# Kernel tuning notes

Measured on AMD Instinct MI355X. Metric: run time of the kernel, lower is better.

## Reference

```python
import jax, jax.numpy as jnp
import numpy as np

WORLD_SIZE = 8
M_LOCAL = 1024   # max_M // world_size
K = 4096
N = 4096


def setup_inputs() -> dict:
    key = jax.random.key(0)
    k1, k2 = jax.random.split(key)
    # Each rank's local activation shard: [world_size, M_local, K]
    A_shards = jax.random.normal(k1, (WORLD_SIZE, M_LOCAL, K), dtype=jnp.float32)
    # weight stored [N, K] (transed_weight = False path)
    weight = jax.random.normal(k2, (N, K), dtype=jnp.float32) * 0.02
    return {"A_shards": A_shards, "weight": weight, "transed_weight": 0}


def reference(A_shards, weight, transed_weight):
    # All-gather: concatenate rank shards along M -> [max_M, K]
    ws, m_local, k = A_shards.shape
    A_full = A_shards.reshape(ws * m_local, k)
    # GEMM: weight is [N, K] when transed_weight is falsy, [K, N] otherwise
    W = weight if transed_weight else weight.T  # -> [K, N]
    out = jnp.matmul(A_full, W)  # [max_M, N]
    return out
```

## Files before the change

### kernel.cpp

```cpp
#include <hip/hip_runtime.h>
#include <hip/hip_bf16.h>

#define M_TOTAL 8192
#define KDIM    4096
#define NDIM    4096

#define BM 256
#define BN 256
#define BK 32
#define NT (KDIM / BK)
#define AREG (BM * BK)
#define BREG (BN * BK)
#define BUFE (AREG + BREG)

typedef __bf16 bf16x8 __attribute__((ext_vector_type(8)));
typedef float  f32x4  __attribute__((ext_vector_type(4)));

__device__ __forceinline__ unsigned short f32_to_bf16_rne(unsigned u) {
    unsigned r = u + 0x7fffu + ((u >> 16) & 1u);
    return (unsigned short)(r >> 16);
}

__device__ __forceinline__ void cvt8(const float* __restrict__ s,
                                     unsigned short* __restrict__ d) {
    const uint4* sp = (const uint4*)s;
    uint4 x = sp[0];
    uint4 y = sp[1];
    uint4 o;
    o.x = (unsigned)f32_to_bf16_rne(x.x) | ((unsigned)f32_to_bf16_rne(x.y) << 16);
    o.y = (unsigned)f32_to_bf16_rne(x.z) | ((unsigned)f32_to_bf16_rne(x.w) << 16);
    o.z = (unsigned)f32_to_bf16_rne(y.x) | ((unsigned)f32_to_bf16_rne(y.y) << 16);
    o.w = (unsigned)f32_to_bf16_rne(y.z) | ((unsigned)f32_to_bf16_rne(y.w) << 16);
    *(uint4*)d = o;
}

__global__ __launch_bounds__(256) void cvt_both(const float* __restrict__ A,
                                                unsigned short* __restrict__ Abf,
                                                long nA,
                                                const float* __restrict__ W,
                                                unsigned short* __restrict__ Wbf) {
    long i = ((long)blockIdx.x * 256 + threadIdx.x) * 8;
    if (i < nA) {
        cvt8(A + i, Abf + i);
    } else {
        long j = i - nA;
        cvt8(W + j, Wbf + j);
    }
}

__device__ __forceinline__ void gload_lds16(const unsigned short* g, unsigned short* l) {
    __builtin_amdgcn_global_load_lds(
        (const __attribute__((address_space(1))) unsigned int*)g,
        (__attribute__((address_space(3))) unsigned int*)l,
        16, 0, 0);
}

__global__ __launch_bounds__(512, 2) void gemm_bt(const unsigned short* __restrict__ A,
                                                  const unsigned short* __restrict__ B,
                                                  float* __restrict__ C) {
    extern __shared__ unsigned short smem[];

    const int tid  = threadIdx.x;
    const int wave = tid >> 6;
    const int lane = tid & 63;

    const int n0 = blockIdx.x * BN;
    const int m0 = blockIdx.y * BM;

    const int rsub = tid >> 2;
    const int cswz = (tid & 3) ^ ((tid >> 3) & 3);
    const unsigned short* pA0 = A + (size_t)(m0 + rsub)       * KDIM + cswz * 8;
    const unsigned short* pA1 = A + (size_t)(m0 + 128 + rsub) * KDIM + cswz * 8;
    const unsigned short* pB0 = B + (size_t)(n0 + rsub)       * KDIM + cswz * 8;
    const unsigned short* pB1 = B + (size_t)(n0 + 128 + rsub) * KDIM + cswz * 8;
    const int woff = wave * 512;

    const int wm   = wave >> 2;
    const int wn   = wave & 3;
    const int quad = lane >> 4;
    const int r    = lane & 15;
    const int sidx = (quad ^ ((r >> 1) & 3)) * 8;

    int aoff[8], boff[4];
#pragma unroll
    for (int mi = 0; mi < 8; ++mi) aoff[mi] = (wm * 128 + mi * 16 + r) * BK + sidx;
#pragma unroll
    for (int ni = 0; ni < 4; ++ni) boff[ni] = (wn * 64 + ni * 16 + r) * BK + sidx;

    f32x4 acc[8][4] = {};

#define SAp(b) (smem + (b) * BUFE)
#define SBq(b) (smem + (b) * BUFE + AREG)
#define STAGE(TS, SB) do {                                                  \
        const size_t so_ = (size_t)(TS) * BK;                               \
        gload_lds16(pA0 + so_, SAp(SB) + woff);                             \
        gload_lds16(pA1 + so_, SAp(SB) + 4096 + woff);                      \
        gload_lds16(pB0 + so_, SBq(SB) + woff);                             \
        gload_lds16(pB1 + so_, SBq(SB) + 4096 + woff);                      \
    } while (0)

    STAGE(0, 0);
    STAGE(1, 1);
    STAGE(2, 2);

#define GITER(RB, SB, VM, DOSTAGE, TS) do {                                 \
        asm volatile("s_waitcnt vmcnt(" #VM ")" ::: "memory");              \
        __builtin_amdgcn_s_barrier();                                       \
        asm volatile("" ::: "memory");                                      \
        if (DOSTAGE) STAGE(TS, SB);                                         \
        bf16x8 aF[8], bF[4];                                                \
        _Pragma("unroll")                                                   \
        for (int mi = 0; mi < 8; ++mi)                                      \
            aF[mi] = *(const bf16x8*)(SAp(RB) + aoff[mi]);                  \
        _Pragma("unroll")                                                   \
        for (int ni = 0; ni < 4; ++ni)                                      \
            bF[ni] = *(const bf16x8*)(SBq(RB) + boff[ni]);                  \
        __builtin_amdgcn_s_setprio(1);                                      \
        _Pragma("unroll")                                                   \
        for (int mi = 0; mi < 8; ++mi)                                      \
            _Pragma("unroll")                                               \
            for (int ni = 0; ni < 4; ++ni)                                  \
                acc[mi][ni] = __builtin_amdgcn_mfma_f32_16x16x32_bf16(      \
                    aF[mi], bF[ni], acc[mi][ni], 0, 0, 0);                  \
        __builtin_amdgcn_s_setprio(0);                                      \
        asm volatile("s_waitcnt lgkmcnt(0)" ::: "memory");                  \
        __builtin_amdgcn_s_barrier();                                       \
        asm volatile("" ::: "memory");                                      \
    } while (0)

    for (int g = 0; g < NT / 4 - 1; ++g) {
        const int t = g * 4;
        GITER(0, 3, 8, true, t + 3);
        GITER(1, 0, 8, true, t + 4);
        GITER(2, 1, 8, true, t + 5);
        GITER(3, 2, 8, true, t + 6);
    }
    GITER(0, 3, 8, true, 127);
    GITER(1, 0, 8, false, 0);
    GITER(2, 1, 4, false, 0);
    GITER(3, 2, 0, false, 0);

#undef GITER
#undef STAGE
#undef SAp
#undef SBq

#pragma unroll
    for (int mi = 0; mi < 8; ++mi) {
        const int row = m0 + wm * 128 + mi * 16 + quad * 4;
#pragma unroll
        for (int ni = 0; ni < 4; ++ni) {
            const int col = n0 + wn * 64 + ni * 16 + r;
            float* p = C + (size_t)row * NDIM + col;
#pragma unroll
            for (int rr = 0; rr < 4; ++rr)
                p[(size_t)rr * NDIM] = acc[mi][ni][rr];
        }
    }
}

extern "C" void kernel_launch(void* const* d_in, const int* in_sizes, int n_in,
                              void* d_out, int out_size, void* d_ws, size_t ws_size,
                              hipStream_t stream) {
    const float* A = (const float*)d_in[0];
    const float* W = (const float*)d_in[1];
    float* out = (float*)d_out;

    unsigned short* Abf = (unsigned short*)d_ws;
    unsigned short* Wbf = Abf + (size_t)M_TOTAL * KDIM;

    const long nA = (long)M_TOTAL * KDIM;
    const long nW = (long)NDIM * KDIM;
    const long nTot = nA + nW;

    cvt_both<<<(int)(nTot / 8 / 256), 256, 0, stream>>>(A, Abf, nA, W, Wbf);

    static bool attr_done = false;
    if (!attr_done) {
        hipFuncSetAttribute((const void*)gemm_bt,
                            hipFuncAttributeMaxDynamicSharedMemorySize, 128 * 1024);
        attr_done = true;
    }

    dim3 grid(NDIM / BN, M_TOTAL / BM);
    gemm_bt<<<grid, 512, 128 * 1024, stream>>>(Abf, Wbf, out);
}
```

Before: 497.5 us.

## Split each K-tile into two half-phases interleaving LDS reads, global loads and MFMAs

Restructures the main loop so each K-step runs as two phases. Each phase loads half of the A fragments, issues half of the next stage's global-to-LDS loads, and runs a 4x4 block of MFMAs, with barriers between phases. The aim is a ping-pong schedule where LDS traffic and global loads overlap with matrix-core work, and fewer fragment registers are live at once. The cost is twice as many barriers per tile and changed vmcnt accounting in the tail, which could cause stalls or a subtle race if the wait counts are wrong.

```diff
diff --git a/kernel.cpp b/kernel.cpp
--- a/kernel.cpp
+++ b/kernel.cpp
@@ -88,6 +88,7 @@
     for (int ni = 0; ni < 4; ++ni) boff[ni] = (wn * 64 + ni * 16 + r) * BK + sidx;
 
     f32x4 acc[8][4] = {};
+    bf16x8 aFa[4], aFb[4], bF[4];
 
 #define SAp(b) (smem + (b) * BUFE)
 #define SBq(b) (smem + (b) * BUFE + AREG)
@@ -99,48 +100,78 @@
         gload_lds16(pB1 + so_, SBq(SB) + 4096 + woff);                      \
     } while (0)
 
+#define TILE(RB, SB, VM, DOSTAGE, TS) do {                                  \
+          \
+        _Pragma("unroll")                                                   \
+        for (int ni = 0; ni < 4; ++ni)                                      \
+            bF[ni] = *(const bf16x8*)(SBq(RB) + boff[ni]);                  \
+        _Pragma("unroll")                                                   \
+        for (int mi = 0; mi < 4; ++mi)                                      \
+            aFa[mi] = *(const bf16x8*)(SAp(RB) + aoff[mi]);                 \
+        if (DOSTAGE) {                                                      \
+            const size_t so_ = (size_t)(TS) * BK;                           \
+            gload_lds16(pA0 + so_, SAp(SB) + woff);                         \
+            gload_lds16(pA1 + so_, SAp(SB) + 4096 + woff);                  \
+        }                                                                   \
+        asm volatile("" ::: "memory");                                      \
+        __builtin_amdgcn_s_barrier();                                       \
+        asm volatile("s_waitcnt lgkmcnt(0)" ::: "memory");                  \
+        __builtin_amdgcn_s_setprio(1);                                      \
+        _Pragma("unroll")                                                   \
+        for (int mi = 0; mi < 4; ++mi)                                      \
+            _Pragma("unroll")                                               \
+            for (int ni = 0; ni < 4; ++ni)                                  \
+                acc[mi][ni] = __builtin_amdgcn_mfma_f32_16x16x32_bf16(      \
+                    aFa[mi], bF[ni], acc[mi][ni], 0, 0, 0);                 \
+        __builtin_amdgcn_s_setprio(0);                                      \
+        asm volatile("" ::: "memory");                                      \
+        __builtin_amdgcn_s_barrier();                                       \
+        asm volatile("" ::: "memory");                                      \
+        \
+        _Pragma("unroll")                                                   \
+        for (int mi = 0; mi < 4; ++mi)                                      \
+            aFb[mi] = *(const bf16x8*)(SAp(RB) + aoff[4 + mi]);             \
+        if (DOSTAGE) {                                                      \
+            const size_t so_ = (size_t)(TS) * BK;                           \
+            gload_lds16(pB0 + so_, SBq(SB) + woff);                         \
+            gload_lds16(pB1 + so_, SBq(SB) + 4096 + woff);                  \
+        }                                                                   \
+        asm volatile("s_waitcnt vmcnt(" #VM ")" ::: "memory");              \
+        __builtin_amdgcn_s_barrier();                                       \
+        asm volatile("s_waitcnt lgkmcnt(0)" ::: "memory");                  \
+        __builtin_amdgcn_s_setprio(1);                                      \
+        _Pragma("unroll")                                                   \
+        for (int mi = 0; mi < 4; ++mi)                                      \
+            _Pragma("unroll")                                               \
+            for (int ni = 0; ni < 4; ++ni)                                  \
+                acc[4 + mi][ni] = __builtin_amdgcn_mfma_f32_16x16x32_bf16(  \
+                    aFb[mi], bF[ni], acc[4 + mi][ni], 0, 0, 0);             \
+        __builtin_amdgcn_s_setprio(0);                                      \
+        asm volatile("" ::: "memory");                                      \
+        __builtin_amdgcn_s_barrier();                                       \
+        asm volatile("" ::: "memory");                                      \
+    } while (0)
+
     STAGE(0, 0);
     STAGE(1, 1);
     STAGE(2, 2);
-
-#define GITER(RB, SB, VM, DOSTAGE, TS) do {                                 \
-        asm volatile("s_waitcnt vmcnt(" #VM ")" ::: "memory");              \
-        __builtin_amdgcn_s_barrier();                                       \
-        asm volatile("" ::: "memory");                                      \
-        if (DOSTAGE) STAGE(TS, SB);                                         \
-        bf16x8 aF[8], bF[4];                                                \
-        _Pragma("unroll")                                                   \
-        for (int mi = 0; mi < 8; ++mi)                                      \
-            aF[mi] = *(const bf16x8*)(SAp(RB) + aoff[mi]);                  \
-        _Pragma("unroll")                                                   \
-        for (int ni = 0; ni < 4; ++ni)                                      \
-            bF[ni] = *(const bf16x8*)(SBq(RB) + boff[ni]);                  \
-        __builtin_amdgcn_s_setprio(1);                                      \
-        _Pragma("unroll")                                                   \
-        for (int mi = 0; mi < 8; ++mi)                                      \
-            _Pragma("unroll")                                               \
-            for (int ni = 0; ni < 4; ++ni)                                  \
-                acc[mi][ni] = __builtin_amdgcn_mfma_f32_16x16x32_bf16(      \
-                    aF[mi], bF[ni], acc[mi][ni], 0, 0, 0);                  \
-        __builtin_amdgcn_s_setprio(0);                                      \
-        asm volatile("s_waitcnt lgkmcnt(0)" ::: "memory");                  \
-        __builtin_amdgcn_s_barrier();                                       \
-        asm volatile("" ::: "memory");                                      \
-    } while (0)
+    asm volatile("s_waitcnt vmcnt(8)" ::: "memory");
+    __builtin_amdgcn_s_barrier();
+    asm volatile("" ::: "memory");
 
     for (int g = 0; g < NT / 4 - 1; ++g) {
         const int t = g * 4;
-        GITER(0, 3, 8, true, t + 3);
-        GITER(1, 0, 8, true, t + 4);
-        GITER(2, 1, 8, true, t + 5);
-        GITER(3, 2, 8, true, t + 6);
-    }
-    GITER(0, 3, 8, true, 127);
-    GITER(1, 0, 8, false, 0);
-    GITER(2, 1, 4, false, 0);
-    GITER(3, 2, 0, false, 0);
-
-#undef GITER
+        TILE(0, 3, 8, true, t + 3);
+        TILE(1, 0, 8, true, t + 4);
+        TILE(2, 1, 8, true, t + 5);
+        TILE(3, 2, 8, true, t + 6);
+    }
+    TILE(0, 3, 8, true, 127);
+    TILE(1, 0, 4, false, 0);
+    TILE(2, 1, 0, false, 0);
+    TILE(3, 2, 0, false, 0);
+
+#undef TILE
 #undef STAGE
 #undef SAp
 #undef SBq
```

After: 486.6 us. 1.02x faster.
